# Performance work log

Measured on AMD Instinct MI355X. Metric: run time of the kernel, lower is better.

Reference implementation:

```python
import jax, jax.numpy as jnp
import numpy as np

M = 100000   # BS*L nodes
D_IN = 256   # in_d
D_OUT = 256  # out_d
E = 1024     # number of edges; indices index the out_d axis (faithful to source quirk)


def setup_inputs() -> dict:
    key = jax.random.key(0)
    k1, k2, k3 = jax.random.split(key, 3)
    node_features = jax.random.normal(k1, (1, M, D_IN), dtype=jnp.float32)
    W = jax.random.normal(k2, (D_OUT, D_IN), dtype=jnp.float32) * (1.0 / np.sqrt(D_IN))
    b = jnp.zeros((D_OUT,), dtype=jnp.float32)
    edge_mapping = jax.random.randint(k3, (2, E), 0, D_OUT, dtype=jnp.int64)
    batch_lens = jnp.ones((M, 1), dtype=jnp.float32)
    return {"node_features": node_features, "W": W, "b": b,
            "edge_mapping": edge_mapping, "batch_lens": batch_lens}


def reference(node_features, W, b, edge_mapping, batch_lens):
    # fc: [1, M, in_d] -> [1, M, out_d]
    h = jnp.einsum('bmi,oi->bmo', node_features, W) + b
    residual = h                              # [1, M, D_OUT]
    hf = jnp.swapaxes(h, 1, 2)[0]             # [D_OUT, M]  (transpose(2,1).squeeze(0))
    gathered = hf[edge_mapping[1]]            # [E, M]      (index_select dim=0)
    agg = jnp.zeros_like(hf).at[edge_mapping[0]].add(gathered)  # scatter-add, [D_OUT, M]
    new_nf = agg.T                            # [M, D_OUT]
    out = (new_nf + residual) / batch_lens    # broadcast -> [1, M, D_OUT]
    return out
```

## Files before the change

### kernel.cpp

```cpp
#include <hip/hip_runtime.h>
#include <cstdint>

constexpr int D = 256;
constexpr int TM = 64;

typedef __bf16 bf16x8 __attribute__((ext_vector_type(8)));
typedef float  f32x4  __attribute__((ext_vector_type(4)));

__global__ void prep_copy(const float* __restrict__ W, const float* __restrict__ b,
                          float* __restrict__ W2, float* __restrict__ b2) {
    int i = blockIdx.x * 256 + threadIdx.x;
    W2[i] = W[i];
    if (blockIdx.x == 0) b2[threadIdx.x] = b[threadIdx.x];
}

__global__ void prep_edges(const int* __restrict__ em, int E,
                           const float* __restrict__ W, const float* __restrict__ b,
                           float* __restrict__ W2, float* __restrict__ b2) {
    int e = blockIdx.x;
    int k = threadIdx.x;
    int dst = em[e];
    int src = em[E + e];
    atomicAdd(&W2[dst * D + k], W[src * D + k]);
    if (k == 0) atomicAdd(&b2[dst], b[src]);
}

__global__ void prep_convert(const float* __restrict__ W2, ushort* __restrict__ Wh,
                             ushort* __restrict__ Wl) {
    int i = blockIdx.x * 256 + threadIdx.x;
    int o = i >> 8, k = i & 255;
    float x = W2[i];
    uint32_t u  = __float_as_uint(x);
    uint32_t hu = u & 0xFFFF0000u;
    float r = x - __uint_as_float(hu);
    uint32_t ru = __float_as_uint(r);
    uint32_t lu = ru + 0x7FFFu + ((ru >> 16) & 1u);
    int kc = k >> 5, kk = k & 31, q = kk >> 3, j = kk & 7;
    int o16b = o >> 4;
    int lane = (o & 15) + 16 * q;
    int idx = kc * 8192 + (o16b * 64 + lane) * 8 + j;
    Wh[idx] = (ushort)(hu >> 16);
    Wl[idx] = (ushort)(lu >> 16);
}

__device__ __forceinline__ void cvt8(const float4& f0, const float4& f1,
                                     uint4& hi, uint4& lo) {
    float xs[8] = {f0.x, f0.y, f0.z, f0.w, f1.x, f1.y, f1.z, f1.w};
    uint32_t h[8], l[8];
    #pragma unroll
    for (int j = 0; j < 8; ++j) {
        uint32_t u  = __float_as_uint(xs[j]);
        uint32_t hu = u & 0xFFFF0000u;
        h[j] = hu;
        float r = xs[j] - __uint_as_float(hu);
        uint32_t ru = __float_as_uint(r);
        l[j] = ru + 0x7FFFu + ((ru >> 16) & 1u);
    }
    hi = make_uint4((h[0] >> 16) | (h[1] & 0xFFFF0000u),
                    (h[2] >> 16) | (h[3] & 0xFFFF0000u),
                    (h[4] >> 16) | (h[5] & 0xFFFF0000u),
                    (h[6] >> 16) | (h[7] & 0xFFFF0000u));
    lo = make_uint4((l[0] >> 16) | (l[1] & 0xFFFF0000u),
                    (l[2] >> 16) | (l[3] & 0xFFFF0000u),
                    (l[4] >> 16) | (l[5] & 0xFFFF0000u),
                    (l[6] >> 16) | (l[7] & 0xFFFF0000u));
}

__global__ __launch_bounds__(256, 3) void resgcn_mfma(
    const float* __restrict__ X, const ushort* __restrict__ Whg,
    const ushort* __restrict__ Wlg, const float* __restrict__ b2,
    const float* __restrict__ blen, float* __restrict__ out, int M)
{
    __shared__ ushort Xh[2][4][64][8];
    __shared__ ushort Xl[2][4][64][8];

    const int tid  = threadIdx.x;
    const int lane = tid & 63;
    const int wv   = tid >> 6;
    const int m0   = blockIdx.x * TM;

    const int sm = tid >> 2;
    const int sh = tid & 3;
    int srow = m0 + sm; if (srow >= M) srow = M - 1;
    const float* xrow = X + (size_t)srow * D + sh * 8;
    const int m16b = sm >> 4;
    const int wlane = (sm & 15) + 16 * sh;

    const ushort* whb = Whg + ((wv * 4) * 64 + lane) * 8;
    const ushort* wlb = Wlg + ((wv * 4) * 64 + lane) * 8;

    f32x4 acc[4][4];
    #pragma unroll
    for (int a = 0; a < 4; ++a)
        #pragma unroll
        for (int b = 0; b < 4; ++b) acc[a][b] = (f32x4){0.f, 0.f, 0.f, 0.f};

    {
        float4 f0 = *(const float4*)(xrow + 0);
        float4 f1 = *(const float4*)(xrow + 4);
        uint4 h, l;
        cvt8(f0, f1, h, l);
        *(uint4*)&Xh[0][m16b][wlane][0] = h;
        *(uint4*)&Xl[0][m16b][wlane][0] = l;
    }
    __syncthreads();

    #pragma unroll 2
    for (int kc = 0; kc < 8; ++kc) {
        const int cur = kc & 1;

        float4 nf0, nf1;
        if (kc < 7) {
            const float* p = xrow + (kc + 1) * 32;
            nf0 = *(const float4*)(p + 0);
            nf1 = *(const float4*)(p + 4);
        }

        bf16x8 bh[4], bl[4];
        #pragma unroll
        for (int b = 0; b < 4; ++b) {
            bh[b] = *(const bf16x8*)(whb + kc * 8192 + b * 512);
            bl[b] = *(const bf16x8*)(wlb + kc * 8192 + b * 512);
        }

        #pragma unroll
        for (int a = 0; a < 4; ++a) {
            bf16x8 ah = *(const bf16x8*)&Xh[cur][a][lane][0];
            bf16x8 al = *(const bf16x8*)&Xl[cur][a][lane][0];
            #pragma unroll
            for (int b = 0; b < 4; ++b) {
                acc[a][b] = __builtin_amdgcn_mfma_f32_16x16x32_bf16(ah, bh[b], acc[a][b], 0, 0, 0);
                acc[a][b] = __builtin_amdgcn_mfma_f32_16x16x32_bf16(al, bh[b], acc[a][b], 0, 0, 0);
                acc[a][b] = __builtin_amdgcn_mfma_f32_16x16x32_bf16(ah, bl[b], acc[a][b], 0, 0, 0);
            }
        }

        if (kc < 7) {
            uint4 h, l;
            cvt8(nf0, nf1, h, l);
            *(uint4*)&Xh[cur ^ 1][m16b][wlane][0] = h;
            *(uint4*)&Xl[cur ^ 1][m16b][wlane][0] = l;
        }
        __syncthreads();
    }

    const int col = lane & 15;
    const int rq  = lane >> 4;
    float bias[4];
    #pragma unroll
    for (int b = 0; b < 4; ++b) bias[b] = b2[(wv * 4 + b) * 16 + col];

    #pragma unroll
    for (int a = 0; a < 4; ++a) {
        #pragma unroll
        for (int r = 0; r < 4; ++r) {
            int m = m0 + a * 16 + rq * 4 + r;
            if (m < M) {
                float inv = 1.0f / blen[m];
                #pragma unroll
                for (int b = 0; b < 4; ++b) {
                    int o = (wv * 4 + b) * 16 + col;
                    out[(size_t)m * D + o] = (acc[a][b][r] + bias[b]) * inv;
                }
            }
        }
    }
}

extern "C" void kernel_launch(void* const* d_in, const int* in_sizes, int n_in,
                              void* d_out, int out_size, void* d_ws, size_t ws_size,
                              hipStream_t stream) {
    (void)n_in; (void)out_size; (void)ws_size;
    const float* X  = (const float*)d_in[0];
    const float* W  = (const float*)d_in[1];
    const float* b  = (const float*)d_in[2];
    const int*   em = (const int*)d_in[3];
    const float* bl = (const float*)d_in[4];
    float* out = (float*)d_out;

    const int M = in_sizes[0] / D;
    const int E = in_sizes[3] / 2;

    float*  W2 = (float*)d_ws;
    float*  b2 = W2 + D * D;
    ushort* Wh = (ushort*)(b2 + D);
    ushort* Wl = Wh + D * D;

    prep_copy<<<D * D / 256, 256, 0, stream>>>(W, b, W2, b2);
    prep_edges<<<E, D, 0, stream>>>(em, E, W, b, W2, b2);
    prep_convert<<<D * D / 256, 256, 0, stream>>>(W2, Wh, Wl);

    int mblocks = (M + TM - 1) / TM;
    resgcn_mfma<<<mblocks, 256, 0, stream>>>(X, Wh, Wl, b2, bl, out, M);
}
```

Before: 224.9 us.

## Double-buffer weight registers and stage epilogue through swizzled LDS for vector stores

The K loop is manually unrolled by two, with ping-pong register sets for the W fragments, so the next chunk's weight loads are issued before the current chunk's MFMAs. The epilogue now writes accumulators into a shared-memory tile with an XOR swizzle, then reads them back so each lane stores a contiguous float4 per output row. This replaces the previous scattered 4-byte stores. The intent is to hide global weight-load latency and to make the output writes, the dominant memory traffic, fully coalesced. The cost is extra registers, which may hurt occupancy at launch bounds of 3, plus added barriers in the epilogue.

```diff
diff --git a/kernel.cpp b/kernel.cpp
--- a/kernel.cpp
+++ b/kernel.cpp
@@ -71,8 +71,10 @@
     const ushort* __restrict__ Wlg, const float* __restrict__ b2,
     const float* __restrict__ blen, float* __restrict__ out, int M)
 {
-    __shared__ ushort Xh[2][4][64][8];
-    __shared__ ushort Xl[2][4][64][8];
+    __shared__ __align__(16) unsigned char smem[16384];
+    ushort* XhP = (ushort*)smem;
+    ushort* XlP = XhP + 4096;
+    float*  E   = (float*)smem;
 
     const int tid  = threadIdx.x;
     const int lane = tid & 63;
@@ -89,59 +91,71 @@
     const ushort* whb = Whg + ((wv * 4) * 64 + lane) * 8;
     const ushort* wlb = Wlg + ((wv * 4) * 64 + lane) * 8;
 
+#define LOADW(BH, BL, c) do {                                             \
+        _Pragma("unroll")                                                 \
+        for (int b = 0; b < 4; ++b) {                                     \
+            BH[b] = *(const bf16x8*)(whb + (c) * 8192 + b * 512);         \
+            BL[b] = *(const bf16x8*)(wlb + (c) * 8192 + b * 512);         \
+        } } while (0)
+
+#define DOMFMA(BH, BL, cur) do {                                          \
+        _Pragma("unroll")                                                 \
+        for (int a = 0; a < 4; ++a) {                                     \
+            bf16x8 ah = *(const bf16x8*)(XhP + (((cur)*4 + a)*64 + lane)*8); \
+            bf16x8 al = *(const bf16x8*)(XlP + (((cur)*4 + a)*64 + lane)*8); \
+            _Pragma("unroll")                                             \
+            for (int b = 0; b < 4; ++b) {                                 \
+                acc[a][b] = __builtin_amdgcn_mfma_f32_16x16x32_bf16(ah, BH[b], acc[a][b], 0, 0, 0); \
+                acc[a][b] = __builtin_amdgcn_mfma_f32_16x16x32_bf16(al, BH[b], acc[a][b], 0, 0, 0); \
+                acc[a][b] = __builtin_amdgcn_mfma_f32_16x16x32_bf16(ah, BL[b], acc[a][b], 0, 0, 0); \
+            } } } while (0)
+
+#define STAGEX(nf0, nf1, buf) do {                                        \
+        uint4 h_, l_;                                                     \
+        cvt8(nf0, nf1, h_, l_);                                           \
+        *(uint4*)(XhP + (((buf)*4 + m16b)*64 + wlane)*8) = h_;            \
+        *(uint4*)(XlP + (((buf)*4 + m16b)*64 + wlane)*8) = l_;            \
+    } while (0)
+
     f32x4 acc[4][4];
     #pragma unroll
     for (int a = 0; a < 4; ++a)
         #pragma unroll
         for (int b = 0; b < 4; ++b) acc[a][b] = (f32x4){0.f, 0.f, 0.f, 0.f};
 
+    bf16x8 bhA[4], blA[4], bhB[4], blB[4];
+    LOADW(bhA, blA, 0);
+
     {
         float4 f0 = *(const float4*)(xrow + 0);
         float4 f1 = *(const float4*)(xrow + 4);
-        uint4 h, l;
-        cvt8(f0, f1, h, l);
-        *(uint4*)&Xh[0][m16b][wlane][0] = h;
-        *(uint4*)&Xl[0][m16b][wlane][0] = l;
+        STAGEX(f0, f1, 0);
     }
     __syncthreads();
 
-    #pragma unroll 2
-    for (int kc = 0; kc < 8; ++kc) {
-        const int cur = kc & 1;
-
-        float4 nf0, nf1;
-        if (kc < 7) {
+    #pragma unroll
+    for (int kc = 0; kc < 8; kc += 2) {
+        {
             const float* p = xrow + (kc + 1) * 32;
-            nf0 = *(const float4*)(p + 0);
-            nf1 = *(const float4*)(p + 4);
-        }
-
-        bf16x8 bh[4], bl[4];
-        #pragma unroll
-        for (int b = 0; b < 4; ++b) {
-            bh[b] = *(const bf16x8*)(whb + kc * 8192 + b * 512);
-            bl[b] = *(const bf16x8*)(wlb + kc * 8192 + b * 512);
-        }
-
-        #pragma unroll
-        for (int a = 0; a < 4; ++a) {
-            bf16x8 ah = *(const bf16x8*)&Xh[cur][a][lane][0];
-            bf16x8 al = *(const bf16x8*)&Xl[cur][a][lane][0];
-            #pragma unroll
-            for (int b = 0; b < 4; ++b) {
-                acc[a][b] = __builtin_amdgcn_mfma_f32_16x16x32_bf16(ah, bh[b], acc[a][b], 0, 0, 0);
-                acc[a][b] = __builtin_amdgcn_mfma_f32_16x16x32_bf16(al, bh[b], acc[a][b], 0, 0, 0);
-                acc[a][b] = __builtin_amdgcn_mfma_f32_16x16x32_bf16(ah, bl[b], acc[a][b], 0, 0, 0);
+            float4 nf0 = *(const float4*)(p + 0);
+            float4 nf1 = *(const float4*)(p + 4);
+            LOADW(bhB, blB, kc + 1);
+            DOMFMA(bhA, blA, 0);
+            STAGEX(nf0, nf1, 1);
+            __syncthreads();
+        }
+        {
+            float4 nf0, nf1;
+            if (kc + 2 < 8) {
+                const float* p = xrow + (kc + 2) * 32;
+                nf0 = *(const float4*)(p + 0);
+                nf1 = *(const float4*)(p + 4);
+                LOADW(bhA, blA, kc + 2);
             }
-        }
-
-        if (kc < 7) {
-            uint4 h, l;
-            cvt8(nf0, nf1, h, l);
-            *(uint4*)&Xh[cur ^ 1][m16b][wlane][0] = h;
-            *(uint4*)&Xl[cur ^ 1][m16b][wlane][0] = l;
-        }
-        __syncthreads();
+            DOMFMA(bhB, blB, 1);
+            if (kc + 2 < 8) STAGEX(nf0, nf1, 0);
+            __syncthreads();
+        }
     }
 
     const int col = lane & 15;
@@ -152,19 +166,33 @@
 
     #pragma unroll
     for (int a = 0; a < 4; ++a) {
+        if (a) __syncthreads();
         #pragma unroll
         for (int r = 0; r < 4; ++r) {
-            int m = m0 + a * 16 + rq * 4 + r;
+            int row = rq * 4 + r;
+            int sw  = (row & 7) << 2;
+            #pragma unroll
+            for (int b = 0; b < 4; ++b) {
+                int o = wv * 64 + b * 16 + col;
+                E[row * 256 + (o ^ sw)] = acc[a][b][r] + bias[b];
+            }
+        }
+        __syncthreads();
+        #pragma unroll
+        for (int j = 0; j < 4; ++j) {
+            int row = wv * 4 + j;
+            int m = m0 + a * 16 + row;
+            f32x4 v = *(const f32x4*)&E[row * 256 + ((lane ^ (row & 7)) << 2)];
             if (m < M) {
                 float inv = 1.0f / blen[m];
-                #pragma unroll
-                for (int b = 0; b < 4; ++b) {
-                    int o = (wv * 4 + b) * 16 + col;
-                    out[(size_t)m * D + o] = (acc[a][b][r] + bias[b]) * inv;
-                }
+                f32x4 o4 = {v[0] * inv, v[1] * inv, v[2] * inv, v[3] * inv};
+                *(f32x4*)&out[(size_t)m * D + lane * 4] = o4;
             }
         }
     }
+#undef LOADW
+#undef DOMFMA
+#undef STAGEX
 }
 
 extern "C" void kernel_launch(void* const* d_in, const int* in_sizes, int n_in,
```

Result: faster. 219.1 us (-2.6%).
